# Kernel optimization log

Measured on AMD Instinct MI355X. Metric: run time of the kernel, lower is better.

Reference implementation:

```python
import jax, jax.numpy as jnp
import numpy as np

DIM = 1024
NUM_HEAD = 8
INNER = DIM // NUM_HEAD
B, L = 2, 2048
EPS = 1e-5  # GroupNorm default eps


def _xavier(key, out_d, in_d, gain=0.01):
    std = gain * np.sqrt(2.0 / (in_d + out_d))
    return (jax.random.normal(key, (out_d, in_d), jnp.float32) * std)


def setup_inputs() -> dict:
    key = jax.random.key(0)
    ks = jax.random.split(key, 12)
    x = jax.random.normal(ks[0], (B, L, DIM), jnp.float32)
    hidden = jax.random.normal(ks[1], (B, NUM_HEAD, INNER), jnp.float32)
    # dt bias: inv-softplus of dt ~ LogUniform(0.001, 0.1), as in __init__
    dt = jnp.exp(jax.random.uniform(ks[2], (NUM_HEAD,), jnp.float32,
                                    minval=np.log(0.001), maxval=np.log(0.1)))
    b_dt = dt + jnp.log1p(-jnp.exp(-dt))
    ln_a = jnp.log(jax.random.uniform(ks[3], (NUM_HEAD,), jnp.float32, minval=1.0, maxval=16.0))
    return {
        "x": x, "hidden": hidden,
        "W_z": _xavier(ks[4], DIM, DIM), "b_z": jnp.zeros((DIM,), jnp.float32),
        "W_z_act": _xavier(ks[5], DIM, DIM), "b_z_act": jnp.zeros((DIM,), jnp.float32),
        "W_y": _xavier(ks[6], DIM, DIM), "b_y": jnp.zeros((DIM,), jnp.float32),
        "W_y_act": _xavier(ks[7], DIM, DIM), "b_y_act": jnp.zeros((DIM,), jnp.float32),
        "W_dt": _xavier(ks[8], NUM_HEAD, DIM), "b_dt": b_dt,
        "ln_a": ln_a,
        "gn_w": jnp.ones((NUM_HEAD,), jnp.float32), "gn_b": jnp.zeros((NUM_HEAD,), jnp.float32),
    }


def reference(x, hidden, W_z, b_z, W_z_act, b_z_act, W_y, b_y, W_y_act, b_y_act,
              W_dt, b_dt, ln_a, gn_w, gn_b):
    b, l, d = x.shape
    nh, inner = NUM_HEAD, d // NUM_HEAD
    silu = jax.nn.silu
    xf = x.astype(jnp.float32)
    # gated input projection -> z: [b,l,h,i]
    z = ((xf @ W_z.T + b_z) * silu(xf @ W_z_act.T + b_z_act)).reshape(b, l, nh, inner)
    # log-decay per step: [b,l,h]
    ln_da = -jnp.exp(ln_a) * jax.nn.softplus(xf @ W_dt.T + b_dt)
    # einops.repeat 'b l h -> b l m h' then torch .tril(-1) (masks over LAST TWO dims (m,h))
    ln_da_masked = jnp.tril(jnp.broadcast_to(ln_da[:, :, None, :], (b, l, l, nh)), k=-1)
    # rfft/irfft conv with ones == prefix sum along l (dim 1)
    ln_da_masked_conv = jnp.cumsum(ln_da_masked, axis=1)
    da_masked_conv = jnp.tril(jnp.exp(ln_da_masked_conv))  # tril over (m,h), k=0
    h_inner = jnp.einsum('blmh,bmhi->blhi', da_masked_conv, z)
    # cross-chunk: cumulative decay applied to carried hidden state
    da_cum = jnp.exp(jnp.cumsum(ln_da, axis=1))  # [b,l,h]
    h_cross = jnp.einsum('blh,bhi->blhi', da_cum, hidden)
    h = h_inner + h_cross  # [b,l,h,i]
    hidden_next = h[:, -1]
    # GroupNorm(num_head groups, num_head channels) on [b*l, h, i]:
    # one channel per group -> normalize over inner dim per (token, head)
    mean = h.mean(axis=-1, keepdims=True)
    var = h.var(axis=-1, keepdims=True)
    h_norm = (h - mean) / jnp.sqrt(var + EPS) * gn_w[None, None, :, None] + gn_b[None, None, :, None]
    h_norm = h_norm.reshape(b, l, d)
    y = (h_norm @ W_y.T + b_y) * silu(xf @ W_y_act.T + b_y_act)
    return y.astype(x.dtype), hidden_next
```

## Files before the change

kernel.cpp:

```cpp
#include <hip/hip_runtime.h>
#include <stdint.h>

#define DIM   1024
#define L_SEQ 2048
#define BATCH 2
#define NH    8
#define M_TOT 4096
#define EPS_F 1e-5f

typedef __bf16 bf16x8 __attribute__((ext_vector_type(8)));
typedef unsigned short u16x8 __attribute__((ext_vector_type(8)));
typedef float f32x4 __attribute__((ext_vector_type(4)));

__device__ __forceinline__ unsigned short f2bf(float f) {
  unsigned int u = __float_as_uint(f);
  u += 0x7FFFu + ((u >> 16) & 1u);
  return (unsigned short)(u >> 16);
}

__device__ __forceinline__ f32x4 mfma_bf16(u16x8 a, u16x8 b, f32x4 c) {
  return __builtin_amdgcn_mfma_f32_16x16x32_bf16(
      __builtin_bit_cast(bf16x8, a), __builtin_bit_cast(bf16x8, b), c, 0, 0, 0);
}

__device__ __forceinline__ float silu_f(float v) {
  return v / (1.f + __expf(-v));
}

__device__ __forceinline__ void gload16(const unsigned short* g, unsigned short* l) {
  __builtin_amdgcn_global_load_lds(
      (const __attribute__((address_space(1))) unsigned int*)g,
      (__attribute__((address_space(3))) unsigned int*)l, 16, 0, 0);
}

__global__ __launch_bounds__(256) void prep_kernel(const float* __restrict__ x,
                                                   const float* __restrict__ W_dt,
                                                   const float* __restrict__ b_dt,
                                                   const float* __restrict__ ln_a,
                                                   const float4* __restrict__ wz,
                                                   const float4* __restrict__ wza,
                                                   const float4* __restrict__ wya,
                                                   float* __restrict__ ln_da,
                                                   unsigned short* __restrict__ xb,
                                                   ushort4* __restrict__ wzb,
                                                   ushort4* __restrict__ wzab,
                                                   ushort4* __restrict__ wyab,
                                                   float* __restrict__ Zs) {
  const int blk = blockIdx.x;
  const int tid = threadIdx.x;
  if (blk >= 4096) {
    const int wb = blk - 4096;
    if (wb < 2) ((f32x4*)Zs)[wb * 256 + tid] = f32x4{0.f, 0.f, 0.f, 0.f};
    int i = wb * 256 + tid;
    const float4* s; ushort4* d; int j;
    if (i < 262144)      { s = wz;  d = wzb;  j = i; }
    else if (i < 524288) { s = wza; d = wzab; j = i - 262144; }
    else                 { s = wya; d = wyab; j = i - 524288; }
    float4 f = s[j];
    d[j] = make_ushort4(f2bf(f.x), f2bf(f.y), f2bf(f.z), f2bf(f.w));
    return;
  }
  __shared__ float xs[DIM];
  const int row = blk;
  float4 f = ((const float4*)(x + (size_t)row * DIM))[tid];
  ((float4*)xs)[tid] = f;
  ((ushort4*)(xb + (size_t)row * DIM))[tid] =
      make_ushort4(f2bf(f.x), f2bf(f.y), f2bf(f.z), f2bf(f.w));
  __syncthreads();
  const int wave = tid >> 6, lane = tid & 63;
  for (int h = wave; h < NH; h += 4) {
    const float* w = W_dt + (size_t)h * DIM;
    float s = 0.f;
    for (int k = lane; k < DIM; k += 64) s += xs[k] * w[k];
    for (int off = 32; off > 0; off >>= 1) s += __shfl_down(s, off);
    if (lane == 0) {
      float t = s + b_dt[h];
      float sp = (t > 20.f) ? t : log1pf(expf(t));
      int b = row >> 11, l = row & (L_SEQ - 1);
      ln_da[(size_t)(b * NH + h) * L_SEQ + l] = -expf(ln_a[h]) * sp;
    }
  }
}

__global__ __launch_bounds__(256, 4) void gemm_all(const unsigned short* __restrict__ xb,
                                                   const unsigned short* __restrict__ Wz,
                                                   const unsigned short* __restrict__ Wza,
                                                   const unsigned short* __restrict__ Wya,
                                                   const float* __restrict__ b_z,
                                                   const float* __restrict__ b_za,
                                                   const float* __restrict__ b_ya,
                                                   float* __restrict__ Zs,
                                                   float* __restrict__ wdiag,
                                                   float* __restrict__ Sy) {
  __shared__ __align__(16) unsigned short As[128 * 64];
  __shared__ __align__(16) unsigned short Bs[128 * 64];
  __shared__ float colsum[64];

  const int tid = threadIdx.x;
  const int lane = tid & 63, wave = tid >> 6;
  const int wm = wave >> 1, wn = wave & 1;
  const int l16 = lane & 15, quad = lane >> 4;
  const int nt = blockIdx.x, mt = blockIdx.y;
  const bool isZ = (nt < 16);
  const int n0 = isZ ? nt * 64 : (nt - 16) * 128;
  const int m0 = mt * 128;

  const int rowl = tid >> 3;
  const int g = (tid & 7) ^ (rowl & 7);
  const size_t aoff = (size_t)(m0 + rowl) * DIM + g * 8;
  const size_t boff = (size_t)(n0 + rowl) * DIM + g * 8;
  const unsigned short* bp0 = isZ ? Wz : Wya;
  const unsigned short* bp1 = isZ ? Wza : (Wya + (size_t)64 * DIM);
  unsigned short* AsD = As + tid * 8;
  unsigned short* BsD = Bs + tid * 8;

  f32x4 acc[4][4];
  const f32x4 zero = {0.f, 0.f, 0.f, 0.f};
  for (int i = 0; i < 4; ++i)
    for (int j = 0; j < 4; ++j) acc[i][j] = zero;

  for (int kt = 0; kt < 16; ++kt) {
    const size_t k0 = (size_t)kt * 64;
    __syncthreads();
    gload16(xb  + aoff + k0,                 AsD);
    gload16(xb  + aoff + 32 * DIM + k0,      AsD + 2048);
    gload16(xb  + aoff + 64 * DIM + k0,      AsD + 4096);
    gload16(xb  + aoff + 96 * DIM + k0,      AsD + 6144);
    gload16(bp0 + boff + k0,                 BsD);
    gload16(bp0 + boff + 32 * DIM + k0,      BsD + 2048);
    gload16(bp1 + boff + k0,                 BsD + 4096);
    gload16(bp1 + boff + 32 * DIM + k0,      BsD + 6144);
    __syncthreads();
#pragma unroll
    for (int kk = 0; kk < 2; ++kk) {
      const int kc = kk * 4 + quad;
      u16x8 aF[4], bF[4];
#pragma unroll
      for (int rb = 0; rb < 4; ++rb) {
        const int r = wm * 64 + rb * 16 + l16;
        aF[rb] = *(const u16x8*)&As[r * 64 + ((kc ^ (r & 7)) << 3)];
      }
#pragma unroll
      for (int cb = 0; cb < 4; ++cb) {
        int r;
        if (isZ) r = (cb < 2) ? (wn * 32 + cb * 16 + l16)
                              : (64 + wn * 32 + (cb - 2) * 16 + l16);
        else     r = wn * 64 + cb * 16 + l16;
        bF[cb] = *(const u16x8*)&Bs[r * 64 + ((kc ^ (r & 7)) << 3)];
      }
#pragma unroll
      for (int rb = 0; rb < 4; ++rb)
#pragma unroll
        for (int cb = 0; cb < 4; ++cb)
          acc[rb][cb] = mfma_bf16(aF[rb], bF[cb], acc[rb][cb]);
    }
  }

  if (isZ) {
    __syncthreads();
    if (tid < 64) colsum[tid] = 0.f;
    __syncthreads();
    const int b = m0 >> 11;
#pragma unroll
    for (int cb = 0; cb < 2; ++cb) {
      const int nl = wn * 32 + cb * 16 + l16;
      const int n = n0 + nl;
      const int h = n >> 7;
      const float bz = b_z[n], ba = b_za[n];
      float ssum = 0.f;
#pragma unroll
      for (int rb = 0; rb < 4; ++rb) {
        const int mlb = wm * 64 + rb * 16 + quad * 4;
#pragma unroll
        for (int r = 0; r < 4; ++r) {
          const int l = (m0 + mlb + r) & (L_SEQ - 1);
          float u  = acc[rb][cb][r] + bz;
          float vv = acc[rb][cb + 2][r] + ba;
          if (l > h) ssum += u * silu_f(vv);
          else if (l == h)
            wdiag[(size_t)(b * NH + h) * 128 + (n & 127)] = u * silu_f(vv);
        }
      }
      atomicAdd(&colsum[nl], ssum);
    }
    __syncthreads();
    if (tid < 64) atomicAdd(&Zs[(size_t)b * DIM + n0 + tid], colsum[tid]);
  } else {
#pragma unroll
    for (int cb = 0; cb < 4; ++cb) {
      const int nl = wn * 64 + cb * 16 + l16;
      const float bb = b_ya[n0 + nl];
#pragma unroll
      for (int rb = 0; rb < 4; ++rb) {
        const int mlb = wm * 64 + rb * 16 + quad * 4;
#pragma unroll
        for (int r = 0; r < 4; ++r)
          Sy[(size_t)(m0 + mlb + r) * DIM + n0 + nl] = silu_f(acc[rb][cb][r] + bb);
      }
    }
  }
}

__global__ __launch_bounds__(256) void stats_scan(const float* __restrict__ Zs,
                                                  const float* __restrict__ hidden,
                                                  const float* __restrict__ wdiag,
                                                  const float* __restrict__ gn_w,
                                                  const float* __restrict__ ln_da,
                                                  float* __restrict__ vtg,
                                                  float* __restrict__ wtg,
                                                  float* __restrict__ alpha2,
                                                  float* __restrict__ hidden_next) {
  const int bh = blockIdx.x, b = bh >> 3, h = bh & 7;
  const int tid = threadIdx.x, wv = tid >> 6, lane = tid & 63;
  __shared__ float csumS[32];
  __shared__ float statS[4];

  float v0 = 0.f, v1 = 0.f, w0 = 0.f, w1 = 0.f;
  const size_t base = (size_t)bh * 128;
  if (wv == 0) {
    v0 = Zs[(size_t)b * DIM + h * 128 + lane]      + hidden[base + lane];
    v1 = Zs[(size_t)b * DIM + h * 128 + 64 + lane] + hidden[base + 64 + lane];
    w0 = wdiag[base + lane];
    w1 = wdiag[base + 64 + lane];
    float sv = v0 + v1, sw = w0 + w1;
    for (int off = 32; off > 0; off >>= 1) {
      sv += __shfl_down(sv, off);
      sw += __shfl_down(sw, off);
    }
    const float muv = __shfl(sv, 0) * (1.f / 128.f);
    const float muw = __shfl(sw, 0) * (1.f / 128.f);
    const float a0 = v0 - muv, a1 = v1 - muv;
    const float c0 = w0 - muw, c1 = w1 - muw;
    float rvv = a0 * a0 + a1 * a1;
    float rvw = a0 * c0 + a1 * c1;
    float rww = c0 * c0 + c1 * c1;
    for (int off = 32; off > 0; off >>= 1) {
      rvv += __shfl_down(rvv, off);
      rvw += __shfl_down(rvw, off);
      rww += __shfl_down(rww, off);
    }
    if (lane == 0) {
      statS[0] = rvv * (1.f / 128.f);
      statS[1] = rvw * (1.f / 128.f);
      statS[2] = rww * (1.f / 128.f);
    }
    const float gw = gn_w[h];
    vtg[base + lane] = a0 * gw;  vtg[base + 64 + lane] = a1 * gw;
    wtg[base + lane] = c0 * gw;  wtg[base + 64 + lane] = c1 * gw;
  }

  const float* src = ln_da + (size_t)bh * L_SEQ;
  float vals[8];
#pragma unroll
  for (int j = 0; j < 8; ++j) {
    const int c = wv * 8 + j;
    float val = src[c * 64 + lane];
#pragma unroll
    for (int off = 1; off < 64; off <<= 1) {
      float nv = __shfl_up(val, off);
      if (lane >= off) val += nv;
    }
    vals[j] = val;
    if (lane == 63) csumS[c] = val;
  }
  __syncthreads();

  if (tid < 32) {
    float s = csumS[tid];
    float incl = s;
#pragma unroll
    for (int off = 1; off < 32; off <<= 1) {
      float nv = __shfl_up(incl, off);
      if (tid >= off) incl += nv;
    }
    csumS[tid] = incl - s;
    if (tid == 31) statS[3] = incl;
  }
  __syncthreads();

  const float svv = statS[0], svw = statS[1], sww = statS[2];
#pragma unroll
  for (int j = 0; j < 8; ++j) {
    const int c = wv * 8 + j;
    const float S = csumS[c] + vals[j];
    const float ce = expf(S);
    const float D = rsqrtf(ce * ce * svv + 2.f * ce * svw + sww + EPS_F);
    const int l = c * 64 + lane;
    float* ap = alpha2 + ((size_t)(b * L_SEQ + l) * NH + h) * 2;
    ap[0] = ce * D;
    ap[1] = D;
  }
  if (wv == 0) {
    const float clast = expf(statS[3]);
    hidden_next[base + lane]      = clast * v0 + w0;
    hidden_next[base + 64 + lane] = clast * v1 + w1;
  }
}

__global__ __launch_bounds__(256) void proj_kernel(const float* __restrict__ W_y,
                                                   const float* __restrict__ vtg,
                                                   const float* __restrict__ wtg,
                                                   const float* __restrict__ gn_b,
                                                   const float* __restrict__ b_y,
                                                   float* __restrict__ Gv,
                                                   float* __restrict__ Gw,
                                                   float* __restrict__ constc) {
  const int tid = threadIdx.x, wave = tid >> 6, lane = tid & 63;
  const int n = blockIdx.x * 4 + wave;
  const float4* row = (const float4*)(W_y + (size_t)n * DIM);
  const int half = lane >> 5, l32 = lane & 31;
  float cc = 0.f;
#pragma unroll
  for (int p = 0; p < 4; ++p) {
    const int h = p * 2 + half;
    float4 wv = row[p * 64 + lane];
    const float4 va = *(const float4*)&vtg[(size_t)h * 128 + l32 * 4];
    const float4 vb = *(const float4*)&vtg[(size_t)(8 + h) * 128 + l32 * 4];
    const float4 wa = *(const float4*)&wtg[(size_t)h * 128 + l32 * 4];
    const float4 wb = *(const float4*)&wtg[(size_t)(8 + h) * 128 + l32 * 4];
    float gv0 = wv.x * va.x + wv.y * va.y + wv.z * va.z + wv.w * va.w;
    float gv1 = wv.x * vb.x + wv.y * vb.y + wv.z * vb.z + wv.w * vb.w;
    float gw0 = wv.x * wa.x + wv.y * wa.y + wv.z * wa.z + wv.w * wa.w;
    float gw1 = wv.x * wb.x + wv.y * wb.y + wv.z * wb.z + wv.w * wb.w;
    cc += (wv.x + wv.y + wv.z + wv.w) * gn_b[h];
#pragma unroll
    for (int off = 16; off > 0; off >>= 1) {
      gv0 += __shfl_down(gv0, off, 32);
      gv1 += __shfl_down(gv1, off, 32);
      gw0 += __shfl_down(gw0, off, 32);
      gw1 += __shfl_down(gw1, off, 32);
    }
    if (l32 == 0) {
      Gv[(size_t)h * DIM + n]       = gv0;
      Gv[(size_t)(8 + h) * DIM + n] = gv1;
      Gw[(size_t)h * DIM + n]       = gw0;
      Gw[(size_t)(8 + h) * DIM + n] = gw1;
    }
  }
  for (int off = 32; off > 0; off >>= 1) cc += __shfl_down(cc, off);
  if (lane == 0) constc[n] = b_y[n] + cc;
}

__global__ __launch_bounds__(256) void finalize(const float* __restrict__ alpha2,
                                                const float* __restrict__ Gv,
                                                const float* __restrict__ Gw,
                                                const float* __restrict__ constc,
                                                float* __restrict__ y) {
  const int tid = threadIdx.x;
  const int n0 = blockIdx.x * 256;
  const int m0 = blockIdx.y * 64;
  const int b = m0 >> 11;
  __shared__ float aS[64 * 16];
  ((float4*)aS)[tid] = ((const float4*)(alpha2 + (size_t)m0 * 16))[tid];
  __syncthreads();
  const int c = tid & 63;
  const int rg = tid >> 6;
  const int n = n0 + c * 4;
  f32x4 g[16 * 2];
#pragma unroll
  for (int h = 0; h < 8; ++h) {
    g[2 * h]     = *(const f32x4*)&Gv[(size_t)(b * NH + h) * DIM + n];
    g[2 * h + 1] = *(const f32x4*)&Gw[(size_t)(b * NH + h) * DIM + n];
  }
  const f32x4 cc = *(const f32x4*)&constc[n];
#pragma unroll
  for (int j = 0; j < 16; ++j) {
    const int m = m0 + rg * 16 + j;
    const float* a = &aS[(rg * 16 + j) * 16];
    f32x4 Ay = cc;
#pragma unroll
    for (int k = 0; k < 16; ++k) Ay += a[k] * g[k];
    f32x4 s = *(const f32x4*)&y[(size_t)m * DIM + n];
    *(f32x4*)&y[(size_t)m * DIM + n] = Ay * s;
  }
}

extern "C" void kernel_launch(void* const* d_in, const int* in_sizes, int n_in,
                              void* d_out, int out_size, void* d_ws, size_t ws_size,
                              hipStream_t stream) {
  const float* x      = (const float*)d_in[0];
  const float* hidden = (const float*)d_in[1];
  const float* W_z    = (const float*)d_in[2];
  const float* b_z    = (const float*)d_in[3];
  const float* W_za   = (const float*)d_in[4];
  const float* b_za   = (const float*)d_in[5];
  const float* W_y    = (const float*)d_in[6];
  const float* b_y    = (const float*)d_in[7];
  const float* W_ya   = (const float*)d_in[8];
  const float* b_ya   = (const float*)d_in[9];
  const float* W_dt   = (const float*)d_in[10];
  const float* b_dt   = (const float*)d_in[11];
  const float* ln_a   = (const float*)d_in[12];
  const float* gn_w   = (const float*)d_in[13];
  const float* gn_b   = (const float*)d_in[14];

  char* ws = (char*)d_ws;
  unsigned short* xb   = (unsigned short*)(ws);
  unsigned short* Wzb  = (unsigned short*)(ws + 8388608);
  unsigned short* Wzab = (unsigned short*)(ws + 10485760);
  unsigned short* Wyab = (unsigned short*)(ws + 12582912);
  float* ln_da  = (float*)(ws + 14680064);
  float* Zs     = (float*)(ws + 14811136);
  float* wdiag  = (float*)(ws + 14819328);
  float* vtg    = (float*)(ws + 14827520);
  float* wtg    = (float*)(ws + 14835712);
  float* Gv     = (float*)(ws + 14843904);
  float* Gw     = (float*)(ws + 14909440);
  float* constc = (float*)(ws + 14974976);
  float* alpha2 = (float*)(ws + 14979072);

  float* y = (float*)d_out;
  float* hidden_next = y + (size_t)M_TOT * DIM;

  prep_kernel<<<7168, 256, 0, stream>>>(x, W_dt, b_dt, ln_a,
                                        (const float4*)W_z, (const float4*)W_za,
                                        (const float4*)W_ya,
                                        ln_da, xb, (ushort4*)Wzb, (ushort4*)Wzab,
                                        (ushort4*)Wyab, Zs);

  gemm_all<<<dim3(24, 32), 256, 0, stream>>>(xb, Wzb, Wzab, Wyab,
                                             b_z, b_za, b_ya, Zs, wdiag, y);

  stats_scan<<<16, 256, 0, stream>>>(Zs, hidden, wdiag, gn_w, ln_da,
                                     vtg, wtg, alpha2, hidden_next);
  proj_kernel<<<256, 256, 0, stream>>>(W_y, vtg, wtg, gn_b, b_y, Gv, Gw, constc);

  finalize<<<dim3(4, 64), 256, 0, stream>>>(alpha2, Gv, Gw, constc, y);
}
```

Measured before the change: 175.0 us.

## Split gate GEMM and fuse finalize into y-activation GEMM epilogue

Separates the z-gate GEMM from the y-activation GEMM and runs the latter after the stats and projection kernels. Its epilogue directly computes the low-rank output term from alpha2, Gv, Gw and constc and multiplies by silu. This removes the intermediate write of silu activations to y and the separate finalize kernel's read-modify-write of the full output. The trade-off is a narrower 64-column tile for the y GEMM, with more A-tile reloads, and a serial ordering that prevents the two GEMMs from sharing one launch.

```diff
diff --git a/kernel.cpp b/kernel.cpp
--- a/kernel.cpp
+++ b/kernel.cpp
@@ -82,16 +82,13 @@
   }
 }
 
-__global__ __launch_bounds__(256, 4) void gemm_all(const unsigned short* __restrict__ xb,
-                                                   const unsigned short* __restrict__ Wz,
-                                                   const unsigned short* __restrict__ Wza,
-                                                   const unsigned short* __restrict__ Wya,
-                                                   const float* __restrict__ b_z,
-                                                   const float* __restrict__ b_za,
-                                                   const float* __restrict__ b_ya,
-                                                   float* __restrict__ Zs,
-                                                   float* __restrict__ wdiag,
-                                                   float* __restrict__ Sy) {
+__global__ __launch_bounds__(256, 4) void gemm_z(const unsigned short* __restrict__ xb,
+                                                 const unsigned short* __restrict__ Wz,
+                                                 const unsigned short* __restrict__ Wza,
+                                                 const float* __restrict__ b_z,
+                                                 const float* __restrict__ b_za,
+                                                 float* __restrict__ Zs,
+                                                 float* __restrict__ wdiag) {
   __shared__ __align__(16) unsigned short As[128 * 64];
   __shared__ __align__(16) unsigned short Bs[128 * 64];
   __shared__ float colsum[64];
@@ -101,16 +98,13 @@
   const int wm = wave >> 1, wn = wave & 1;
   const int l16 = lane & 15, quad = lane >> 4;
   const int nt = blockIdx.x, mt = blockIdx.y;
-  const bool isZ = (nt < 16);
-  const int n0 = isZ ? nt * 64 : (nt - 16) * 128;
+  const int n0 = nt * 64;
   const int m0 = mt * 128;
 
   const int rowl = tid >> 3;
   const int g = (tid & 7) ^ (rowl & 7);
   const size_t aoff = (size_t)(m0 + rowl) * DIM + g * 8;
   const size_t boff = (size_t)(n0 + rowl) * DIM + g * 8;
-  const unsigned short* bp0 = isZ ? Wz : Wya;
-  const unsigned short* bp1 = isZ ? Wza : (Wya + (size_t)64 * DIM);
   unsigned short* AsD = As + tid * 8;
   unsigned short* BsD = Bs + tid * 8;
 
@@ -122,14 +116,14 @@
   for (int kt = 0; kt < 16; ++kt) {
     const size_t k0 = (size_t)kt * 64;
     __syncthreads();
-    gload16(xb  + aoff + k0,                 AsD);
-    gload16(xb  + aoff + 32 * DIM + k0,      AsD + 2048);
-    gload16(xb  + aoff + 64 * DIM + k0,      AsD + 4096);
-    gload16(xb  + aoff + 96 * DIM + k0,      AsD + 6144);
-    gload16(bp0 + boff + k0,                 BsD);
-    gload16(bp0 + boff + 32 * DIM + k0,      BsD + 2048);
-    gload16(bp1 + boff + k0,                 BsD + 4096);
-    gload16(bp1 + boff + 32 * DIM + k0,      BsD + 6144);
+    gload16(xb  + aoff + k0,                AsD);
+    gload16(xb  + aoff + 32 * DIM + k0,     AsD + 2048);
+    gload16(xb  + aoff + 64 * DIM + k0,     AsD + 4096);
+    gload16(xb  + aoff + 96 * DIM + k0,     AsD + 6144);
+    gload16(Wz  + boff + k0,                BsD);
+    gload16(Wz  + boff + 32 * DIM + k0,     BsD + 2048);
+    gload16(Wza + boff + k0,                BsD + 4096);
+    gload16(Wza + boff + 32 * DIM + k0,     BsD + 6144);
     __syncthreads();
 #pragma unroll
     for (int kk = 0; kk < 2; ++kk) {
@@ -142,10 +136,8 @@
       }
 #pragma unroll
       for (int cb = 0; cb < 4; ++cb) {
-        int r;
-        if (isZ) r = (cb < 2) ? (wn * 32 + cb * 16 + l16)
-                              : (64 + wn * 32 + (cb - 2) * 16 + l16);
-        else     r = wn * 64 + cb * 16 + l16;
+        const int r = (cb < 2) ? (wn * 32 + cb * 16 + l16)
+                               : (64 + wn * 32 + (cb - 2) * 16 + l16);
         bF[cb] = *(const u16x8*)&Bs[r * 64 + ((kc ^ (r & 7)) << 3)];
       }
 #pragma unroll
@@ -156,49 +148,34 @@
     }
   }
 
-  if (isZ) {
-    __syncthreads();
-    if (tid < 64) colsum[tid] = 0.f;
-    __syncthreads();
-    const int b = m0 >> 11;
-#pragma unroll
-    for (int cb = 0; cb < 2; ++cb) {
-      const int nl = wn * 32 + cb * 16 + l16;
-      const int n = n0 + nl;
-      const int h = n >> 7;
-      const float bz = b_z[n], ba = b_za[n];
-      float ssum = 0.f;
-#pragma unroll
-      for (int rb = 0; rb < 4; ++rb) {
-        const int mlb = wm * 64 + rb * 16 + quad * 4;
-#pragma unroll
-        for (int r = 0; r < 4; ++r) {
-          const int l = (m0 + mlb + r) & (L_SEQ - 1);
-          float u  = acc[rb][cb][r] + bz;
-          float vv = acc[rb][cb + 2][r] + ba;
-          if (l > h) ssum += u * silu_f(vv);
-          else if (l == h)
-            wdiag[(size_t)(b * NH + h) * 128 + (n & 127)] = u * silu_f(vv);
-        }
-      }
-      atomicAdd(&colsum[nl], ssum);
-    }
-    __syncthreads();
-    if (tid < 64) atomicAdd(&Zs[(size_t)b * DIM + n0 + tid], colsum[tid]);
-  } else {
-#pragma unroll
-    for (int cb = 0; cb < 4; ++cb) {
-      const int nl = wn * 64 + cb * 16 + l16;
-      const float bb = b_ya[n0 + nl];
-#pragma unroll
-      for (int rb = 0; rb < 4; ++rb) {
-        const int mlb = wm * 64 + rb * 16 + quad * 4;
-#pragma unroll
-        for (int r = 0; r < 4; ++r)
-          Sy[(size_t)(m0 + mlb + r) * DIM + n0 + nl] = silu_f(acc[rb][cb][r] + bb);
-      }
-    }
-  }
+  __syncthreads();
+  if (tid < 64) colsum[tid] = 0.f;
+  __syncthreads();
+  const int b = m0 >> 11;
+#pragma unroll
+  for (int cb = 0; cb < 2; ++cb) {
+    const int nl = wn * 32 + cb * 16 + l16;
+    const int n = n0 + nl;
+    const int h = n >> 7;
+    const float bz = b_z[n], ba = b_za[n];
+    float ssum = 0.f;
+#pragma unroll
+    for (int rb = 0; rb < 4; ++rb) {
+      const int mlb = wm * 64 + rb * 16 + quad * 4;
+#pragma unroll
+      for (int r = 0; r < 4; ++r) {
+        const int l = (m0 + mlb + r) & (L_SEQ - 1);
+        float u  = acc[rb][cb][r] + bz;
+        float vv = acc[rb][cb + 2][r] + ba;
+        if (l > h) ssum += u * silu_f(vv);
+        else if (l == h)
+          wdiag[(size_t)(b * NH + h) * 128 + (n & 127)] = u * silu_f(vv);
+      }
+    }
+    atomicAdd(&colsum[nl], ssum);
+  }
+  __syncthreads();
+  if (tid < 64) atomicAdd(&Zs[(size_t)b * DIM + n0 + tid], colsum[tid]);
 }
 
 __global__ __launch_bounds__(256) void stats_scan(const float* __restrict__ Zs,
@@ -341,37 +318,106 @@
   if (lane == 0) constc[n] = b_y[n] + cc;
 }
 
-__global__ __launch_bounds__(256) void finalize(const float* __restrict__ alpha2,
-                                                const float* __restrict__ Gv,
-                                                const float* __restrict__ Gw,
-                                                const float* __restrict__ constc,
-                                                float* __restrict__ y) {
+__global__ __launch_bounds__(256, 4) void gemm_y(const unsigned short* __restrict__ xb,
+                                                 const unsigned short* __restrict__ Wya,
+                                                 const float* __restrict__ b_ya,
+                                                 const float* __restrict__ alpha2,
+                                                 const float* __restrict__ Gv,
+                                                 const float* __restrict__ Gw,
+                                                 const float* __restrict__ constc,
+                                                 float* __restrict__ y) {
+  __shared__ __align__(16) unsigned short As[128 * 64];
+  __shared__ __align__(16) unsigned short Bs[64 * 64];
+  __shared__ float cS[64];
+  __shared__ float bS[64];
+
   const int tid = threadIdx.x;
-  const int n0 = blockIdx.x * 256;
-  const int m0 = blockIdx.y * 64;
+  const int lane = tid & 63, wave = tid >> 6;
+  const int wm = wave >> 1, wn = wave & 1;
+  const int l16 = lane & 15, quad = lane >> 4;
+  const int nt = blockIdx.x, mt = blockIdx.y;
+  const int n0 = nt * 64;
+  const int m0 = mt * 128;
   const int b = m0 >> 11;
-  __shared__ float aS[64 * 16];
-  ((float4*)aS)[tid] = ((const float4*)(alpha2 + (size_t)m0 * 16))[tid];
-  __syncthreads();
-  const int c = tid & 63;
-  const int rg = tid >> 6;
-  const int n = n0 + c * 4;
-  f32x4 g[16 * 2];
-#pragma unroll
-  for (int h = 0; h < 8; ++h) {
-    g[2 * h]     = *(const f32x4*)&Gv[(size_t)(b * NH + h) * DIM + n];
-    g[2 * h + 1] = *(const f32x4*)&Gw[(size_t)(b * NH + h) * DIM + n];
-  }
-  const f32x4 cc = *(const f32x4*)&constc[n];
-#pragma unroll
-  for (int j = 0; j < 16; ++j) {
-    const int m = m0 + rg * 16 + j;
-    const float* a = &aS[(rg * 16 + j) * 16];
-    f32x4 Ay = cc;
-#pragma unroll
-    for (int k = 0; k < 16; ++k) Ay += a[k] * g[k];
-    f32x4 s = *(const f32x4*)&y[(size_t)m * DIM + n];
-    *(f32x4*)&y[(size_t)m * DIM + n] = Ay * s;
+
+  const int rowl = tid >> 3;
+  const int g = (tid & 7) ^ (rowl & 7);
+  const size_t aoff = (size_t)(m0 + rowl) * DIM + g * 8;
+  const size_t boff = (size_t)(n0 + rowl) * DIM + g * 8;
+  unsigned short* AsD = As + tid * 8;
+  unsigned short* BsD = Bs + tid * 8;
+
+  f32x4 acc[4][2];
+  const f32x4 zero = {0.f, 0.f, 0.f, 0.f};
+  for (int i = 0; i < 4; ++i)
+    for (int j = 0; j < 2; ++j) acc[i][j] = zero;
+
+  for (int kt = 0; kt < 16; ++kt) {
+    const size_t k0 = (size_t)kt * 64;
+    __syncthreads();
+    gload16(xb  + aoff + k0,                AsD);
+    gload16(xb  + aoff + 32 * DIM + k0,     AsD + 2048);
+    gload16(xb  + aoff + 64 * DIM + k0,     AsD + 4096);
+    gload16(xb  + aoff + 96 * DIM + k0,     AsD + 6144);
+    gload16(Wya + boff + k0,                BsD);
+    gload16(Wya + boff + 32 * DIM + k0,     BsD + 2048);
+    __syncthreads();
+#pragma unroll
+    for (int kk = 0; kk < 2; ++kk) {
+      const int kc = kk * 4 + quad;
+      u16x8 aF[4], bF[2];
+#pragma unroll
+      for (int rb = 0; rb < 4; ++rb) {
+        const int r = wm * 64 + rb * 16 + l16;
+        aF[rb] = *(const u16x8*)&As[r * 64 + ((kc ^ (r & 7)) << 3)];
+      }
+#pragma unroll
+      for (int cb = 0; cb < 2; ++cb) {
+        const int r = wn * 32 + cb * 16 + l16;
+        bF[cb] = *(const u16x8*)&Bs[r * 64 + ((kc ^ (r & 7)) << 3)];
+      }
+#pragma unroll
+      for (int rb = 0; rb < 4; ++rb)
+#pragma unroll
+        for (int cb = 0; cb < 2; ++cb)
+          acc[rb][cb] = mfma_bf16(aF[rb], bF[cb], acc[rb][cb]);
+    }
+  }
+
+  __syncthreads();
+  float* aS = (float*)As;
+  float* gS = (float*)Bs;
+  {
+    const float4* ap = (const float4*)(alpha2 + (size_t)m0 * 16);
+    ((float4*)aS)[tid] = ap[tid];
+    ((float4*)aS)[256 + tid] = ap[256 + tid];
+    for (int i = tid; i < 16 * 64; i += 256) {
+      const int k = i >> 6, n = i & 63, h = k >> 1;
+      const float* src = (k & 1) ? Gw : Gv;
+      gS[i] = src[(size_t)(b * NH + h) * DIM + n0 + n];
+    }
+    if (tid < 64) { cS[tid] = constc[n0 + tid]; bS[tid] = b_ya[n0 + tid]; }
+  }
+  __syncthreads();
+
+#pragma unroll
+  for (int cb = 0; cb < 2; ++cb) {
+    const int nl = wn * 32 + cb * 16 + l16;
+    const float bb = bS[nl];
+    const float cc = cS[nl];
+#pragma unroll
+    for (int rb = 0; rb < 4; ++rb) {
+      const int mlb = wm * 64 + rb * 16 + quad * 4;
+#pragma unroll
+      for (int r = 0; r < 4; ++r) {
+        const int ml = mlb + r;
+        const float* a = &aS[ml * 16];
+        float Ay = cc;
+#pragma unroll
+        for (int k = 0; k < 16; ++k) Ay += a[k] * gS[k * 64 + nl];
+        y[(size_t)(m0 + ml) * DIM + n0 + nl] = Ay * silu_f(acc[rb][cb][r] + bb);
+      }
+    }
   }
 }
 
@@ -418,12 +464,11 @@
                                         ln_da, xb, (ushort4*)Wzb, (ushort4*)Wzab,
                                         (ushort4*)Wyab, Zs);
 
-  gemm_all<<<dim3(24, 32), 256, 0, stream>>>(xb, Wzb, Wzab, Wyab,
-                                             b_z, b_za, b_ya, Zs, wdiag, y);
+  gemm_z<<<dim3(16, 32), 256, 0, stream>>>(xb, Wzb, Wzab, b_z, b_za, Zs, wdiag);
 
   stats_scan<<<16, 256, 0, stream>>>(Zs, hidden, wdiag, gn_w, ln_da,
                                      vtg, wtg, alpha2, hidden_next);
   proj_kernel<<<256, 256, 0, stream>>>(W_y, vtg, wtg, gn_b, b_y, Gv, Gw, constc);
 
-  finalize<<<dim3(4, 64), 256, 0, stream>>>(alpha2, Gv, Gw, constc, y);
-}
+  gemm_y<<<dim3(16, 32), 256, 0, stream>>>(xb, Wyab, b_ya, alpha2, Gv, Gw, constc, y);
+}
```

Result: slower. 190.6 us (+8.9%).
